# Performance work log

Hardware: AMD Instinct MI355X
Metric: run time of the kernel (lower is better)

The kernel has to match this reference:

```python
import jax, jax.numpy as jnp
import numpy as np

N = 50000      # nodes
E = 800000     # edges (avg degree 16)
F_IN = 256     # input feature dim
H = 4          # heads
D = 16         # out feats per head
NEG_SLOPE = 0.2


def setup_inputs() -> dict:
    key = jax.random.key(0)
    ks = jax.random.split(key, 8)
    feat = jax.random.normal(ks[0], (N, F_IN), dtype=jnp.float32)
    src = jax.random.randint(ks[1], (E,), 0, N, dtype=jnp.int32)
    dst = jax.random.randint(ks[2], (E,), 0, N, dtype=jnp.int32)
    sc = 1.0 / np.sqrt(F_IN)
    W_src = (jax.random.normal(ks[3], (H * D, F_IN), dtype=jnp.float32) * sc)
    b_src = jnp.zeros((H * D,), dtype=jnp.float32)
    W_dst = (jax.random.normal(ks[4], (H * D, F_IN), dtype=jnp.float32) * sc)
    b_dst = jnp.zeros((H * D,), dtype=jnp.float32)
    attn = jax.random.normal(ks[5], (1, H, D), dtype=jnp.float32) * (1.0 / np.sqrt(D))
    return {"feat": feat, "src": src, "dst": dst, "W_src": W_src,
            "b_src": b_src, "W_dst": W_dst, "b_dst": b_dst, "attn": attn}


def reference(feat, src, dst, W_src, b_src, W_dst, b_dst, attn):
    # Dense projections: [N, H, D]
    feat_src = (feat @ W_src.T + b_src).reshape(N, H, D)
    feat_dst = (feat @ W_dst.T + b_dst).reshape(N, H, D)
    # Gather to edges: [E, H, D]
    el = feat_src[src]
    er = feat_dst[dst]
    e = jax.nn.leaky_relu(el + er, negative_slope=NEG_SLOPE)
    # Per-edge, per-head attention logit: [E, H]
    score = jnp.einsum('ehd,ohd->eh', e, attn)
    # Edge softmax over incoming edges of each destination node
    m = jax.ops.segment_max(score, dst, num_segments=N)          # [N, H]
    a = jnp.exp(score - m[dst])                                  # [E, H]
    s = jax.ops.segment_sum(a, dst, num_segments=N)              # [N, H]
    alpha = a / s[dst]                                           # [E, H]
    # Weighted scatter-aggregate of source features: [N, H, D]
    msg = el * alpha[:, :, None]
    rst = jax.ops.segment_sum(msg, dst, num_segments=N)
    return rst
```

## Files before the change

kernel.cpp:

```cpp
#include <hip/hip_runtime.h>
#include <math.h>

#define NODES 50000
#define EDGES 800000
#define FIN   256
#define HD    64
#define NEG   0.2f

#define PROJ_BLOCKS 782
#define NB          196
#define STAGE_BLOCKS 196
#define PREP_BLOCKS 128
#define HIST_BLOCKS 3125

typedef __attribute__((ext_vector_type(8))) short bf16x8;
typedef __attribute__((ext_vector_type(4))) float f32x4;

__device__ __forceinline__ unsigned pack_hi(unsigned a, unsigned b)
{ return (a >> 16) | (b & 0xFFFF0000u); }

__device__ __forceinline__ void split8(const float4 x01, const float4 x23,
                                       bf16x8& hi, bf16x8& lo)
{
    const float xs[8] = { x01.x, x01.y, x01.z, x01.w, x23.x, x23.y, x23.z, x23.w };
    union { unsigned w[4]; bf16x8 v; } H, L;
#pragma unroll
    for (int p = 0; p < 4; ++p) {
        const float a = xs[2 * p], b = xs[2 * p + 1];
        const unsigned ba = __float_as_uint(a), bb = __float_as_uint(b);
        H.w[p] = pack_hi(ba, bb);
        const float la = a - __uint_as_float(ba & 0xFFFF0000u);
        const float lb = b - __uint_as_float(bb & 0xFFFF0000u);
        L.w[p] = pack_hi(__float_as_uint(la), __float_as_uint(lb));
    }
    hi = H.v; lo = L.v;
}

__global__ void prep_hist_kernel(const float* __restrict__ Wsrc,
                                 const float* __restrict__ Wdst,
                                 short* __restrict__ Bhi, short* __restrict__ Blo,
                                 const int* __restrict__ dst, int* __restrict__ deg)
{
    const int b = blockIdx.x;
    if (b < PREP_BLOCKS) {
        const int i = b * 256 + threadIdx.x;
        const int row = i >> 8, k = i & 255;
        const float x = (row < 64) ? Wsrc[row * FIN + k] : Wdst[(row - 64) * FIN + k];
        const unsigned bb = __float_as_uint(x);
        const float l = x - __uint_as_float(bb & 0xFFFF0000u);
        Bhi[i] = (short)(bb >> 16);
        Blo[i] = (short)(__float_as_uint(l) >> 16);
    } else {
        const int e = (b - PREP_BLOCKS) * 256 + threadIdx.x;
        if (e < EDGES) atomicAdd(&deg[dst[e]], 1);
    }
}

__global__ void scan1_kernel(const int* __restrict__ deg, int* __restrict__ offs,
                             int* __restrict__ part)
{
    __shared__ int lds[256];
    const int t  = threadIdx.x;
    const int i0 = blockIdx.x * 1024 + t * 4;
    int v[4];
#pragma unroll
    for (int k = 0; k < 4; ++k) v[k] = (i0 + k < NODES) ? deg[i0 + k] : 0;
    const int tsum = v[0] + v[1] + v[2] + v[3];
    lds[t] = tsum;
    __syncthreads();
    for (int off = 1; off < 256; off <<= 1) {
        const int x = (t >= off) ? lds[t - off] : 0;
        __syncthreads();
        lds[t] += x;
        __syncthreads();
    }
    const int excl = lds[t] - tsum;
    int run = excl;
#pragma unroll
    for (int k = 0; k < 4; ++k) {
        if (i0 + k < NODES) offs[i0 + k] = run;
        run += v[k];
    }
    if (t == 255) part[blockIdx.x] = lds[255];
}

__global__ void scan3_kernel(int* __restrict__ offs, const int* __restrict__ part,
                             int* __restrict__ bcur)
{
    const int i = blockIdx.x * blockDim.x + threadIdx.x;
    const int pidx = blockIdx.x >> 2;
    int add = 0;
    for (int b = 0; b < pidx; ++b) add += part[b];
    if (i < NODES) {
        const int val = offs[i] + add;
        offs[i] = val;
        if ((i & 255) == 0) bcur[i >> 8] = val;
    }
    if (i == 0) offs[NODES] = EDGES;
}

__global__ __launch_bounds__(256) void proj_stage_kernel(
    const float* __restrict__ feat,
    const short* __restrict__ Bhi, const short* __restrict__ Blo,
    const float* __restrict__ bsrc, const float* __restrict__ bdst,
    float* __restrict__ fs, float* __restrict__ fd,
    const int* __restrict__ src, const int* __restrict__ dst,
    int* __restrict__ bcur, unsigned* __restrict__ bedge)
{
    __shared__ short sB[2][2][512 * 8];
    __shared__ int   sH[NB], sBase[NB];

    const int t = threadIdx.x;

    if (blockIdx.x >= PROJ_BLOCKS) {
        const int e0 = (blockIdx.x - PROJ_BLOCKS) * 4096;
        for (int i = t; i < NB; i += 256) sH[i] = 0;
        __syncthreads();
#pragma unroll
        for (int k = 0; k < 16; ++k) {
            const int e = e0 + k * 256 + t;
            if (e < EDGES) atomicAdd(&sH[dst[e] >> 8], 1);
        }
        __syncthreads();
        for (int i = t; i < NB; i += 256) {
            const int c = sH[i];
            sBase[i] = c ? atomicAdd(&bcur[i], c) : 0;
            sH[i] = 0;
        }
        __syncthreads();
#pragma unroll
        for (int k = 0; k < 16; ++k) {
            const int e = e0 + k * 256 + t;
            if (e < EDGES) {
                const int d = dst[e];
                const int b = d >> 8;
                const int p = sBase[b] + atomicAdd(&sH[b], 1);
                bedge[p] = (unsigned)src[e] | ((unsigned)(d & 255) << 16);
            }
        }
        return;
    }

    const int lane = t & 63;
    const int w    = t >> 6;
    const int fr   = lane & 15;
    const int fq   = lane >> 4;
    const int fragu = fq * 128 + fr;

    const int colu = t & 127;
    const int fq0  = t >> 7;
    const int fq1  = fq0 + 2;

    const int r0 = blockIdx.x * 64 + w * 16;
    int rowA = r0 + fr;  if (rowA >= NODES) rowA = NODES - 1;
    const float* pA = feat + (size_t)rowA * FIN + fq * 8;

    f32x4 acc[8];
#pragma unroll
    for (int n = 0; n < 8; ++n) acc[n] = (f32x4){0.f, 0.f, 0.f, 0.f};

    float4 bs00, bs01, bs10, bs11;
    float4 acA, acB, anA, anB;

#define B_ISSUE(kslice) do {                                                  \
        const size_t o0 = (size_t)colu * FIN + (kslice) * 32 + fq0 * 8;       \
        const size_t o1 = (size_t)colu * FIN + (kslice) * 32 + fq1 * 8;       \
        bs00 = *(const float4*)(Bhi + o0);  bs01 = *(const float4*)(Bhi + o1);\
        bs10 = *(const float4*)(Blo + o0);  bs11 = *(const float4*)(Blo + o1);\
    } while (0)

#define B_WRITE(buf) do {                                                     \
        *(float4*)&sB[buf][0][(size_t)t * 8]         = bs00;                  \
        *(float4*)&sB[buf][0][(size_t)(t + 256) * 8] = bs01;                  \
        *(float4*)&sB[buf][1][(size_t)t * 8]         = bs10;                  \
        *(float4*)&sB[buf][1][(size_t)(t + 256) * 8] = bs11;                  \
    } while (0)

#define A_LOAD(dA, dB, kslice) do {                                           \
        dA = *(const float4*)(pA + (kslice) * 32);                            \
        dB = *(const float4*)(pA + (kslice) * 32 + 4);                        \
    } while (0)

#define COMPUTE(buf, AH, AL) do {                                             \
        _Pragma("unroll")                                                     \
        for (int nf = 0; nf < 8; ++nf) {                                      \
            const bf16x8 bh = *(const bf16x8*)&sB[buf][0][(fragu + nf*16)*8]; \
            const bf16x8 bl = *(const bf16x8*)&sB[buf][1][(fragu + nf*16)*8]; \
            acc[nf] = __builtin_amdgcn_mfma_f32_16x16x32_bf16(AH, bh, acc[nf], 0, 0, 0); \
            acc[nf] = __builtin_amdgcn_mfma_f32_16x16x32_bf16(AL, bh, acc[nf], 0, 0, 0); \
            acc[nf] = __builtin_amdgcn_mfma_f32_16x16x32_bf16(AH, bl, acc[nf], 0, 0, 0); \
        } } while (0)

    B_ISSUE(0);
    A_LOAD(acA, acB, 0);
    B_WRITE(0);
    __syncthreads();

    for (int ks2 = 0; ks2 < 8; ks2 += 2) {
        const int k1 = (ks2 + 1 < 7) ? ks2 + 1 : 7;
        const int k2 = (ks2 + 2 < 7) ? ks2 + 2 : 7;
        bf16x8 ah, al;

        B_ISSUE(k1);
        A_LOAD(anA, anB, k1);
        split8(acA, acB, ah, al);
        COMPUTE(0, ah, al);
        B_WRITE(1);
        __syncthreads();

        B_ISSUE(k2);
        A_LOAD(acA, acB, k2);
        split8(anA, anB, ah, al);
        COMPUTE(1, ah, al);
        B_WRITE(0);
        __syncthreads();
    }

#pragma unroll
    for (int nf = 0; nf < 8; ++nf) {
        float* outp = (nf < 4) ? fs : fd;
        const float bias = ((nf < 4) ? bsrc : bdst)[(nf & 3) * 16 + fr];
        const int c = (nf & 3) * 16 + fr;
#pragma unroll
        for (int r = 0; r < 4; ++r) {
            const int row = r0 + fq * 4 + r;
            if (row < NODES)
                outp[(size_t)row * HD + c] = acc[nf][r] + bias;
        }
    }
#undef B_ISSUE
#undef B_WRITE
#undef A_LOAD
#undef COMPUTE
}

__global__ __launch_bounds__(256) void bucket_scatter_kernel(
    const int* __restrict__ offs, const unsigned* __restrict__ bedge,
    unsigned short* __restrict__ csr)
{
    __shared__ int cur[256];
    const int b  = blockIdx.x;
    const int t  = threadIdx.x;
    const int n0 = b * 256;
    const int start = offs[n0];
    const int node  = n0 + t;
    cur[t] = ((node < NODES) ? offs[node] : EDGES) - start;
    __syncthreads();
    const int end = (n0 + 256 <= NODES) ? offs[n0 + 256] : EDGES;
    for (int i = start + t; i < end; i += 256) {
        const unsigned pk = bedge[i];
        const int rel = atomicAdd(&cur[(pk >> 16) & 255], 1);
        csr[start + rel] = (unsigned short)(pk & 0xFFFFu);
    }
}

__device__ __forceinline__ float head_sum16(float x)
{
    x += __int_as_float(__builtin_amdgcn_update_dpp(0, __float_as_int(x), 0xB1,  0xf, 0xf, true));
    x += __int_as_float(__builtin_amdgcn_update_dpp(0, __float_as_int(x), 0x4E,  0xf, 0xf, true));
    x += __int_as_float(__builtin_amdgcn_update_dpp(0, __float_as_int(x), 0x141, 0xf, 0xf, true));
    x += __int_as_float(__builtin_amdgcn_update_dpp(0, __float_as_int(x), 0x140, 0xf, 0xf, true));
    return x;
}

__global__ __launch_bounds__(256) void gat_kernel(
    const float* __restrict__ fs, const float* __restrict__ fd,
    const float* __restrict__ attn,
    const int* __restrict__ offs, const unsigned short* __restrict__ csr,
    float* __restrict__ out)
{
    const int wid  = (blockIdx.x * blockDim.x + threadIdx.x) >> 6;
    const int lane = threadIdx.x & 63;
    if (wid >= NODES) return;

    const float er = fd[(size_t)wid * HD + lane];
    const float aw = attn[lane];
    const int start = __builtin_amdgcn_readfirstlane(offs[wid]);
    const int end   = __builtin_amdgcn_readfirstlane(offs[wid + 1]);

    float s = 0.f, acc = 0.f;

    for (int base = start; base < end; base += 64) {
        const int rem = end - base;
        const int cnt = rem < 64 ? rem : 64;
        int srcv = 0;
        if (lane < cnt) srcv = (int)csr[base + lane];

        int j = 0;
        for (; j + 4 <= cnt; j += 4) {
            const int i0 = __builtin_amdgcn_readlane(srcv, j + 0);
            const int i1 = __builtin_amdgcn_readlane(srcv, j + 1);
            const int i2 = __builtin_amdgcn_readlane(srcv, j + 2);
            const int i3 = __builtin_amdgcn_readlane(srcv, j + 3);
            const float el0 = fs[(size_t)i0 * HD + lane];
            const float el1 = fs[(size_t)i1 * HD + lane];
            const float el2 = fs[(size_t)i2 * HD + lane];
            const float el3 = fs[(size_t)i3 * HD + lane];
            const float t0 = el0 + er, t1 = el1 + er, t2 = el2 + er, t3 = el3 + er;
            const float e0 = fmaf(NEG, fminf(t0, 0.f), fmaxf(t0, 0.f));
            const float e1 = fmaf(NEG, fminf(t1, 0.f), fmaxf(t1, 0.f));
            const float e2 = fmaf(NEG, fminf(t2, 0.f), fmaxf(t2, 0.f));
            const float e3 = fmaf(NEG, fminf(t3, 0.f), fmaxf(t3, 0.f));
            const float p0 = head_sum16(e0 * aw);
            const float p1 = head_sum16(e1 * aw);
            const float p2 = head_sum16(e2 * aw);
            const float p3 = head_sum16(e3 * aw);
            const float pe0 = __expf(p0);
            const float pe1 = __expf(p1);
            const float pe2 = __expf(p2);
            const float pe3 = __expf(p3);
            s += (pe0 + pe1) + (pe2 + pe3);
            acc = fmaf(pe0, el0, fmaf(pe1, el1, fmaf(pe2, el2, fmaf(pe3, el3, acc))));
        }
        for (; j < cnt; ++j) {
            const int i0 = __builtin_amdgcn_readlane(srcv, j);
            const float el0 = fs[(size_t)i0 * HD + lane];
            const float t0 = el0 + er;
            const float e0 = fmaf(NEG, fminf(t0, 0.f), fmaxf(t0, 0.f));
            const float pe0 = __expf(head_sum16(e0 * aw));
            s += pe0;
            acc = fmaf(pe0, el0, acc);
        }
    }
    out[(size_t)wid * HD + lane] = (end > start) ? (acc / s) : 0.f;
}

extern "C" void kernel_launch(void* const* d_in, const int* in_sizes, int n_in,
                              void* d_out, int out_size, void* d_ws, size_t ws_size,
                              hipStream_t stream)
{
    const float* feat = (const float*)d_in[0];
    const int*   src  = (const int*)  d_in[1];
    const int*   dst  = (const int*)  d_in[2];
    const float* Wsrc = (const float*)d_in[3];
    const float* bsrc = (const float*)d_in[4];
    const float* Wdst = (const float*)d_in[5];
    const float* bdst = (const float*)d_in[6];
    const float* attn = (const float*)d_in[7];
    float* out = (float*)d_out;

    float* fs     = (float*)d_ws;
    float* fd     = fs + (size_t)NODES * HD;
    int*   offs   = (int*)(fd + (size_t)NODES * HD);
    int*   deg    = offs + (NODES + 16);
    int*   part   = deg + NODES;
    int*   bcur   = part + 64;
    unsigned* bedge = (unsigned*)(bcur + 256);
    unsigned short* csr = (unsigned short*)(bedge + EDGES);
    short* Bhi    = (short*)(csr + EDGES);
    short* Blo    = Bhi + 128 * FIN;

    const int scan_blocks = (NODES + 1023) / 1024;

    hipMemsetAsync(deg, 0, NODES * sizeof(int), stream);

    prep_hist_kernel<<<PREP_BLOCKS + HIST_BLOCKS, 256, 0, stream>>>(
        Wsrc, Wdst, Bhi, Blo, dst, deg);
    scan1_kernel<<<scan_blocks, 256, 0, stream>>>(deg, offs, part);
    scan3_kernel<<<(NODES + 255) / 256, 256, 0, stream>>>(offs, part, bcur);
    proj_stage_kernel<<<PROJ_BLOCKS + STAGE_BLOCKS, 256, 0, stream>>>(
        feat, Bhi, Blo, bsrc, bdst, fs, fd, src, dst, bcur, bedge);
    bucket_scatter_kernel<<<NB, 256, 0, stream>>>(offs, bedge, csr);
    gat_kernel<<<((size_t)NODES * 64 + 255) / 256, 256, 0, stream>>>(
        fs, fd, attn, offs, csr, out);
}
```

Before: 223.5 us.

## Replace per-node degree histogram and scan with bucket-level counts and in-bucket scan

Drops the per-node degree histogram built with global atomics over 800k edges, along with the two-kernel scan over 50k nodes. It is replaced by LDS-aggregated counts for each 256-node bucket, a single-block bucket scan, and a per-node offset scan computed inside the bucket scatter kernel. This removes one launch, shrinks the memset, and cuts global atomic contention, at the cost of an extra pass over bedge in the scatter kernel. It also restructures the projection k-loop into a fully unrolled loop with a 3-deep A-register prefetch ring.

```diff
diff --git a/kernel.cpp b/kernel.cpp
--- a/kernel.cpp
+++ b/kernel.cpp
@@ -11,7 +11,6 @@
 #define NB          196
 #define STAGE_BLOCKS 196
 #define PREP_BLOCKS 128
-#define HIST_BLOCKS 3125
 
 typedef __attribute__((ext_vector_type(8))) short bf16x8;
 typedef __attribute__((ext_vector_type(4))) float f32x4;
@@ -36,67 +35,57 @@
     hi = H.v; lo = L.v;
 }
 
-__global__ void prep_hist_kernel(const float* __restrict__ Wsrc,
-                                 const float* __restrict__ Wdst,
-                                 short* __restrict__ Bhi, short* __restrict__ Blo,
-                                 const int* __restrict__ dst, int* __restrict__ deg)
+__global__ void prep_count_kernel(const float* __restrict__ Wsrc,
+                                  const float* __restrict__ Wdst,
+                                  short* __restrict__ Bhi, short* __restrict__ Blo,
+                                  const int* __restrict__ dst, int* __restrict__ bcnt)
 {
     const int b = blockIdx.x;
+    const int t = threadIdx.x;
     if (b < PREP_BLOCKS) {
-        const int i = b * 256 + threadIdx.x;
+        const int i = b * 256 + t;
         const int row = i >> 8, k = i & 255;
         const float x = (row < 64) ? Wsrc[row * FIN + k] : Wdst[(row - 64) * FIN + k];
         const unsigned bb = __float_as_uint(x);
         const float l = x - __uint_as_float(bb & 0xFFFF0000u);
         Bhi[i] = (short)(bb >> 16);
         Blo[i] = (short)(__float_as_uint(l) >> 16);
-    } else {
-        const int e = (b - PREP_BLOCKS) * 256 + threadIdx.x;
-        if (e < EDGES) atomicAdd(&deg[dst[e]], 1);
-    }
-}
-
-__global__ void scan1_kernel(const int* __restrict__ deg, int* __restrict__ offs,
-                             int* __restrict__ part)
-{
-    __shared__ int lds[256];
-    const int t  = threadIdx.x;
-    const int i0 = blockIdx.x * 1024 + t * 4;
-    int v[4];
-#pragma unroll
-    for (int k = 0; k < 4; ++k) v[k] = (i0 + k < NODES) ? deg[i0 + k] : 0;
-    const int tsum = v[0] + v[1] + v[2] + v[3];
-    lds[t] = tsum;
+        return;
+    }
+    __shared__ int sH[NB];
+    for (int i = t; i < NB; i += 256) sH[i] = 0;
+    __syncthreads();
+    const int e0 = (b - PREP_BLOCKS) * 4096;
+#pragma unroll
+    for (int k = 0; k < 16; ++k) {
+        const int e = e0 + k * 256 + t;
+        if (e < EDGES) atomicAdd(&sH[dst[e] >> 8], 1);
+    }
+    __syncthreads();
+    for (int i = t; i < NB; i += 256) {
+        const int c = sH[i];
+        if (c) atomicAdd(&bcnt[i], c);
+    }
+}
+
+__global__ void bscan_kernel(const int* __restrict__ bcnt, int* __restrict__ bbase,
+                             int* __restrict__ bcur, int* __restrict__ offs)
+{
+    __shared__ int s[256];
+    const int t = threadIdx.x;
+    const int v = (t < NB) ? bcnt[t] : 0;
+    s[t] = v;
     __syncthreads();
     for (int off = 1; off < 256; off <<= 1) {
-        const int x = (t >= off) ? lds[t - off] : 0;
-        __syncthreads();
-        lds[t] += x;
-        __syncthreads();
-    }
-    const int excl = lds[t] - tsum;
-    int run = excl;
-#pragma unroll
-    for (int k = 0; k < 4; ++k) {
-        if (i0 + k < NODES) offs[i0 + k] = run;
-        run += v[k];
-    }
-    if (t == 255) part[blockIdx.x] = lds[255];
-}
-
-__global__ void scan3_kernel(int* __restrict__ offs, const int* __restrict__ part,
-                             int* __restrict__ bcur)
-{
-    const int i = blockIdx.x * blockDim.x + threadIdx.x;
-    const int pidx = blockIdx.x >> 2;
-    int add = 0;
-    for (int b = 0; b < pidx; ++b) add += part[b];
-    if (i < NODES) {
-        const int val = offs[i] + add;
-        offs[i] = val;
-        if ((i & 255) == 0) bcur[i >> 8] = val;
-    }
-    if (i == 0) offs[NODES] = EDGES;
+        const int x = (t >= off) ? s[t - off] : 0;
+        __syncthreads();
+        s[t] += x;
+        __syncthreads();
+    }
+    const int excl = s[t] - v;
+    if (t <= NB) bbase[t] = excl;
+    if (t < NB)  bcur[t]  = excl;
+    if (t == 0)  offs[NODES] = EDGES;
 }
 
 __global__ __launch_bounds__(256) void proj_stage_kernel(
@@ -160,7 +149,7 @@
     for (int n = 0; n < 8; ++n) acc[n] = (f32x4){0.f, 0.f, 0.f, 0.f};
 
     float4 bs00, bs01, bs10, bs11;
-    float4 acA, acB, anA, anB;
+    float4 aR[3][2];
 
 #define B_ISSUE(kslice) do {                                                  \
         const size_t o0 = (size_t)colu * FIN + (kslice) * 32 + fq0 * 8;       \
@@ -176,9 +165,9 @@
         *(float4*)&sB[buf][1][(size_t)(t + 256) * 8] = bs11;                  \
     } while (0)
 
-#define A_LOAD(dA, dB, kslice) do {                                           \
-        dA = *(const float4*)(pA + (kslice) * 32);                            \
-        dB = *(const float4*)(pA + (kslice) * 32 + 4);                        \
+#define A_LD(r, kslice) do {                                                  \
+        aR[r][0] = *(const float4*)(pA + (kslice) * 32);                      \
+        aR[r][1] = *(const float4*)(pA + (kslice) * 32 + 4);                  \
     } while (0)
 
 #define COMPUTE(buf, AH, AL) do {                                             \
@@ -192,27 +181,20 @@
         } } while (0)
 
     B_ISSUE(0);
-    A_LOAD(acA, acB, 0);
+    A_LD(0, 0);
+    A_LD(1, 1);
     B_WRITE(0);
     __syncthreads();
 
-    for (int ks2 = 0; ks2 < 8; ks2 += 2) {
-        const int k1 = (ks2 + 1 < 7) ? ks2 + 1 : 7;
-        const int k2 = (ks2 + 2 < 7) ? ks2 + 2 : 7;
+#pragma unroll
+    for (int ks = 0; ks < 8; ++ks) {
+        const int buf = ks & 1;
+        if (ks < 7) B_ISSUE(ks + 1);
+        if (ks < 6) A_LD((ks + 2) % 3, ks + 2);
         bf16x8 ah, al;
-
-        B_ISSUE(k1);
-        A_LOAD(anA, anB, k1);
-        split8(acA, acB, ah, al);
-        COMPUTE(0, ah, al);
-        B_WRITE(1);
-        __syncthreads();
-
-        B_ISSUE(k2);
-        A_LOAD(acA, acB, k2);
-        split8(anA, anB, ah, al);
-        COMPUTE(1, ah, al);
-        B_WRITE(0);
+        split8(aR[ks % 3][0], aR[ks % 3][1], ah, al);
+        COMPUTE(buf, ah, al);
+        if (ks < 7) B_WRITE(buf ^ 1);
         __syncthreads();
     }
 
@@ -230,26 +212,45 @@
     }
 #undef B_ISSUE
 #undef B_WRITE
-#undef A_LOAD
+#undef A_LD
 #undef COMPUTE
 }
 
 __global__ __launch_bounds__(256) void bucket_scatter_kernel(
-    const int* __restrict__ offs, const unsigned* __restrict__ bedge,
-    unsigned short* __restrict__ csr)
-{
-    __shared__ int cur[256];
-    const int b  = blockIdx.x;
-    const int t  = threadIdx.x;
-    const int n0 = b * 256;
-    const int start = offs[n0];
-    const int node  = n0 + t;
-    cur[t] = ((node < NODES) ? offs[node] : EDGES) - start;
-    __syncthreads();
-    const int end = (n0 + 256 <= NODES) ? offs[n0 + 256] : EDGES;
+    const int* __restrict__ bbase, const unsigned* __restrict__ bedge,
+    int* __restrict__ offs, unsigned short* __restrict__ csr)
+{
+    __shared__ int s[256];
+    __shared__ int pl[256];
+    const int b = blockIdx.x;
+    const int t = threadIdx.x;
+    const int start = bbase[b];
+    const int end   = bbase[b + 1];
+
+    s[t] = 0;
+    __syncthreads();
+    for (int i = start + t; i < end; i += 256)
+        atomicAdd(&s[(bedge[i] >> 16) & 255], 1);
+    __syncthreads();
+
+    const int v = s[t];
+    __syncthreads();
+    for (int off = 1; off < 256; off <<= 1) {
+        const int x = (t >= off) ? s[t - off] : 0;
+        __syncthreads();
+        s[t] += x;
+        __syncthreads();
+    }
+    const int excl = s[t] - v;
+
+    const int node = b * 256 + t;
+    if (node < NODES) offs[node] = start + excl;
+    pl[t] = excl;
+    __syncthreads();
+
     for (int i = start + t; i < end; i += 256) {
         const unsigned pk = bedge[i];
-        const int rel = atomicAdd(&cur[(pk >> 16) & 255], 1);
+        const int rel = atomicAdd(&pl[(pk >> 16) & 255], 1);
         csr[start + rel] = (unsigned short)(pk & 0xFFFFu);
     }
 }
@@ -342,25 +343,22 @@
     float* fs     = (float*)d_ws;
     float* fd     = fs + (size_t)NODES * HD;
     int*   offs   = (int*)(fd + (size_t)NODES * HD);
-    int*   deg    = offs + (NODES + 16);
-    int*   part   = deg + NODES;
-    int*   bcur   = part + 64;
+    int*   bcnt   = offs + (NODES + 16);
+    int*   bbase  = bcnt + 256;
+    int*   bcur   = bbase + 256;
     unsigned* bedge = (unsigned*)(bcur + 256);
     unsigned short* csr = (unsigned short*)(bedge + EDGES);
     short* Bhi    = (short*)(csr + EDGES);
     short* Blo    = Bhi + 128 * FIN;
 
-    const int scan_blocks = (NODES + 1023) / 1024;
-
-    hipMemsetAsync(deg, 0, NODES * sizeof(int), stream);
-
-    prep_hist_kernel<<<PREP_BLOCKS + HIST_BLOCKS, 256, 0, stream>>>(
-        Wsrc, Wdst, Bhi, Blo, dst, deg);
-    scan1_kernel<<<scan_blocks, 256, 0, stream>>>(deg, offs, part);
-    scan3_kernel<<<(NODES + 255) / 256, 256, 0, stream>>>(offs, part, bcur);
+    hipMemsetAsync(bcnt, 0, 256 * sizeof(int), stream);
+
+    prep_count_kernel<<<PREP_BLOCKS + STAGE_BLOCKS, 256, 0, stream>>>(
+        Wsrc, Wdst, Bhi, Blo, dst, bcnt);
+    bscan_kernel<<<1, 256, 0, stream>>>(bcnt, bbase, bcur, offs);
     proj_stage_kernel<<<PROJ_BLOCKS + STAGE_BLOCKS, 256, 0, stream>>>(
         feat, Bhi, Blo, bsrc, bdst, fs, fd, src, dst, bcur, bedge);
-    bucket_scatter_kernel<<<NB, 256, 0, stream>>>(offs, bedge, csr);
+    bucket_scatter_kernel<<<NB, 256, 0, stream>>>(bbase, bedge, offs, csr);
     gat_kernel<<<((size_t)NODES * 64 + 255) / 256, 256, 0, stream>>>(
         fs, fd, attn, offs, csr, out);
 }
```

After: 194.6 us. -12.9%, faster.
